# Optimization experiments

Measured on AMD Instinct MI355X. Metric: run time of the kernel, lower is better.

## Reference

```python
import jax, jax.numpy as jnp
import numpy as np

BS, NQ, NC = 8, 100, 81      # batch, queries, classes (COCO-like)
M = 160                      # total targets across batch (20 per image)
H = W = 256                  # mask resolution
P = H * W                    # pixels per mask

COST_CLASS = 1.0
COST_MASK = 1.0
COST_DICE = 1.0


def setup_inputs() -> dict:
    key = jax.random.key(0)
    k1, k2, k3, k4 = jax.random.split(key, 4)
    return {
        "pred_logits": jax.random.normal(k1, (BS, NQ, NC), dtype=jnp.float32),
        "pred_masks": jax.random.normal(k2, (BS, NQ, H, W), dtype=jnp.float32),
        "tgt_ids": jax.random.randint(k3, (M,), 0, NC),
        # binary ground-truth masks, flattened to [M, P]
        "tgt_mask": jnp.round(jax.random.uniform(k4, (M, P), dtype=jnp.float32)),
    }


def reference(pred_logits, pred_masks, tgt_ids, tgt_mask):
    bs, nq = pred_logits.shape[:2]
    N = bs * nq

    # ---- classification cost: -softmax(logits)[:, tgt_ids]  -> [N, M]
    out_prob = jax.nn.softmax(pred_logits.reshape(N, -1), axis=-1)
    cost_class = -out_prob[:, tgt_ids]

    x = pred_masks.reshape(N, -1)          # [N, P] mask logits
    t = tgt_mask                           # [M, P] binary targets
    p = x.shape[1]

    # ---- pairwise BCE-with-logits cost, mean over pixels.
    # bce(x, t) = max(x,0) - x*t + log1p(exp(-|x|)); mean_p splits into a
    # per-prediction row term minus a matmul cross term (avoids the N x M x P blowup).
    pos = jnp.maximum(x, 0.0) + jnp.log1p(jnp.exp(-jnp.abs(x)))   # [N, P]
    row = pos.sum(axis=1)                                          # [N]
    cross = x @ t.T                                                # [N, M]
    cost_mask = (row[:, None] - cross) / p

    # ---- pairwise dice cost: 1 - (2<s,t> + 1) / (sum s + sum t + 1)
    s = jax.nn.sigmoid(x)                                          # [N, P]
    numerator = 2.0 * (s @ t.T)                                    # [N, M]
    denominator = s.sum(axis=1)[:, None] + t.sum(axis=1)[None, :]  # [N, M]
    cost_dice = 1.0 - (numerator + 1.0) / (denominator + 1.0)

    C = COST_CLASS * cost_class + COST_MASK * cost_mask + COST_DICE * cost_dice
    return C.reshape(bs, nq, -1)           # [bs, nq, M] cost matrix
```

## Files before the change

### kernel.cpp

```cpp
#include <hip/hip_runtime.h>
#include <cmath>

#define NROWS 800
#define NCLS  81
#define MT    160
#define PPX   65536
#define SSPLIT 32
#define CHUNK 2048
#define BK    64
#define ITERS (CHUNK / BK)
#define RPB   32
#define RB    25

#define OFF_TBF   0
#define SZ_TBF    (MT * PPX * 2)
#define OFF_CROSS (SZ_TBF)
#define OFF_SDOT  (OFF_CROSS + NROWS * MT * 4)
#define OFF_ROW   (OFF_SDOT + NROWS * MT * 4)
#define OFF_SSUM  (OFF_ROW + NROWS * 4)
#define OFF_TSUM  (OFF_SSUM + NROWS * 4)
#define OFF_PROB  (OFF_TSUM + MT * 4)
#define OFF_END   (OFF_PROB + NROWS * NCLS * 4)

typedef __attribute__((ext_vector_type(8))) short bf16x8;
typedef __attribute__((ext_vector_type(4))) float f32x4;

typedef __attribute__((address_space(3))) char lds_char;
typedef const __attribute__((address_space(1))) char glob_char;

__device__ __forceinline__ unsigned short f2bf(float f) {
    unsigned int u = __float_as_uint(f);
    unsigned int r = (u + 0x7FFFu + ((u >> 16) & 1u)) >> 16;
    return (unsigned short)r;
}

__global__ __launch_bounds__(256) void prep_kernel(const float* __restrict__ tgt_mask,
                                                   char* __restrict__ ws) {
    int g = blockIdx.x * 256 + threadIdx.x;
    int m = g >> 13;
    int kc = g & 8191;
    const float4* src = (const float4*)(tgt_mask + (size_t)m * PPX + (kc << 3));
    float4 a = src[0], b = src[1];
    float part = a.x + a.y + a.z + a.w + b.x + b.y + b.z + b.w;

    uint4 o;
    o.x = (unsigned)f2bf(a.x) | ((unsigned)f2bf(a.y) << 16);
    o.y = (unsigned)f2bf(a.z) | ((unsigned)f2bf(a.w) << 16);
    o.z = (unsigned)f2bf(b.x) | ((unsigned)f2bf(b.y) << 16);
    o.w = (unsigned)f2bf(b.z) | ((unsigned)f2bf(b.w) << 16);

    int group = kc >> 3;
    int c = kc & 7;
    int oc = (group << 3) | (c ^ (m & 7));
    *(uint4*)(ws + OFF_TBF + (size_t)m * (PPX * 2) + (size_t)oc * 16) = o;

    #pragma unroll
    for (int mk = 32; mk; mk >>= 1) part += __shfl_xor(part, mk);
    __shared__ float wsum[4];
    if ((threadIdx.x & 63) == 0) wsum[threadIdx.x >> 6] = part;
    __syncthreads();
    if (threadIdx.x == 0) {
        float tot = wsum[0] + wsum[1] + wsum[2] + wsum[3];
        atomicAdd((float*)(ws + OFF_TSUM) + m, tot);
    }
}

__global__ __launch_bounds__(64) void softmax_kernel(const float* __restrict__ logits,
                                                     float* __restrict__ prob) {
    int n = blockIdx.x;
    int l = threadIdx.x;
    const float* row = logits + n * NCLS;
    float v0 = row[l];
    float v1 = (l + 64 < NCLS) ? row[l + 64] : -INFINITY;
    float mx = fmaxf(v0, v1);
    #pragma unroll
    for (int mk = 32; mk; mk >>= 1) mx = fmaxf(mx, __shfl_xor(mx, mk));
    float e0 = __expf(v0 - mx);
    float e1 = (l + 64 < NCLS) ? __expf(v1 - mx) : 0.f;
    float s = e0 + e1;
    #pragma unroll
    for (int mk = 32; mk; mk >>= 1) s += __shfl_xor(s, mk);
    float inv = 1.f / s;
    prob[n * NCLS + l] = e0 * inv;
    if (l + 64 < NCLS) prob[n * NCLS + l + 64] = e1 * inv;
}

struct XS { float4 a; float4 b; };

__device__ __forceinline__ void loadx(XS& x, const float* xrow, int it) {
    const float* p = xrow + it * BK;
    x.a = *(const float4*)(p);
    x.b = *(const float4*)(p + 4);
}

__device__ __forceinline__ void ew8(const XS& xs, bf16x8& xv, bf16x8& sv,
                                    float& slog2, float& sg_acc) {
    float vals[8] = {xs.a.x, xs.a.y, xs.a.z, xs.a.w, xs.b.x, xs.b.y, xs.b.z, xs.b.w};
    #pragma unroll
    for (int j = 0; j < 8; ++j) {
        float v = vals[j];
        float vl = fminf(v * 1.44269504089f, 126.f);
        float t2 = __builtin_amdgcn_exp2f(vl);
        float d = 1.f + t2;
        float r = __builtin_amdgcn_rcpf(d);
        float sg = t2 * r;
        slog2 += __builtin_amdgcn_logf(d);
        sg_acc += sg;
        xv[j] = (short)f2bf(v);
        sv[j] = (short)f2bf(sg);
    }
}

__global__ __launch_bounds__(256) void main_kernel(const float* __restrict__ pred_masks,
                                                   char* __restrict__ ws) {
    __shared__ __align__(16) unsigned short lds_t[2][MT * BK];
    __shared__ __align__(16) unsigned short lds_x[RPB * BK];
    __shared__ __align__(16) unsigned short lds_s[RPB * BK];

    const int tid = threadIdx.x;
    const int w = tid >> 6, l = tid & 63;
    const int rb = blockIdx.x >> 5;
    const int s = blockIdx.x & 31;
    const int k_base = s * CHUNK;

    const int srow = tid >> 3;
    const int sc8 = tid & 7;
    const int n_glob = rb * RPB + srow;
    const float* xrow = pred_masks + (size_t)n_glob * PPX + k_base + sc8 * 8;
    char* xw = (char*)lds_x + srow * 128 + ((sc8 ^ (srow & 7)) * 16);
    char* swp = (char*)lds_s + srow * 128 + ((sc8 ^ (srow & 7)) * 16);

    const char* tbase = ws + OFF_TBF;

    auto stage_t = [&](int b, int tt) {
        const int k0 = k_base + tt * BK;
        #pragma unroll
        for (int i = 0; i < 5; ++i) {
            int rows_base = w * 40 + i * 8;
            const char* g = (const char*)tbase
                          + (size_t)(rows_base + (l >> 3)) * (PPX * 2)
                          + (size_t)k0 * 2 + (size_t)(l & 7) * 16;
            __builtin_amdgcn_global_load_lds((glob_char*)g,
                                             (lds_char*)((char*)lds_t[b] + rows_base * 128),
                                             16, 0, 0);
        }
    };

    const int wr = w & 1, wc = w >> 1;
    f32x4 accX[5], accS[5];
    #pragma unroll
    for (int i = 0; i < 5; ++i) { accX[i] = (f32x4)(0.f); accS[i] = (f32x4)(0.f); }
    float slog2 = 0.f, rs_sg = 0.f;

    stage_t(0, 0);
    XS XA, XB;
    loadx(XA, xrow, 0);
    loadx(XB, xrow, 1);

    #pragma unroll 1
    for (int it = 0; it < ITERS; it += 2) {
        #pragma unroll
        for (int half = 0; half < 2; ++half) {
            const int h = it + half;
            const int hb = half;

            int tn = h + 1; if (tn >= ITERS) tn = ITERS - 1;
            stage_t(hb ^ 1, tn);
            __builtin_amdgcn_sched_barrier(0);

            bf16x8 xv, sv;
            if (half == 0) ew8(XA, xv, sv, slog2, rs_sg);
            else           ew8(XB, xv, sv, slog2, rs_sg);
            *(bf16x8*)xw = xv;
            *(bf16x8*)swp = sv;

            int tr = h + 2; if (tr >= ITERS) tr = ITERS - 1;
            if (half == 0) loadx(XA, xrow, tr);
            else           loadx(XB, xrow, tr);

            asm volatile("s_waitcnt vmcnt(9) lgkmcnt(0)" ::: "memory");
            __builtin_amdgcn_sched_barrier(0);
            __builtin_amdgcn_s_barrier();
            __builtin_amdgcn_sched_barrier(0);

            #pragma unroll
            for (int kk = 0; kk < 2; ++kk) {
                int arow = wr * 16 + (l & 15);
                int achunk = (kk * 4 + (l >> 4)) ^ (arow & 7);
                bf16x8 ax = *(bf16x8*)((char*)lds_x + arow * 128 + achunk * 16);
                bf16x8 as = *(bf16x8*)((char*)lds_s + arow * 128 + achunk * 16);
                #pragma unroll
                for (int cf = 0; cf < 5; ++cf) {
                    int mrow = (wc * 5 + cf) * 16 + (l & 15);
                    int bchunk = (kk * 4 + (l >> 4)) ^ (mrow & 7);
                    bf16x8 bv = *(bf16x8*)((char*)lds_t[hb] + mrow * 128 + bchunk * 16);
                    accX[cf] = __builtin_amdgcn_mfma_f32_16x16x32_bf16(ax, bv, accX[cf], 0, 0, 0);
                    accS[cf] = __builtin_amdgcn_mfma_f32_16x16x32_bf16(as, bv, accS[cf], 0, 0, 0);
                }
            }

            asm volatile("s_waitcnt lgkmcnt(0)" ::: "memory");
            __builtin_amdgcn_sched_barrier(0);
            __builtin_amdgcn_s_barrier();
            __builtin_amdgcn_sched_barrier(0);
        }
    }

    asm volatile("s_waitcnt vmcnt(0)" ::: "memory");

    float rs_sp = slog2 * 0.69314718056f;
    rs_sp += __shfl_xor(rs_sp, 1); rs_sp += __shfl_xor(rs_sp, 2); rs_sp += __shfl_xor(rs_sp, 4);
    rs_sg += __shfl_xor(rs_sg, 1); rs_sg += __shfl_xor(rs_sg, 2); rs_sg += __shfl_xor(rs_sg, 4);
    float* acc_row = (float*)(ws + OFF_ROW);
    float* acc_ssum = (float*)(ws + OFF_SSUM);
    if ((tid & 7) == 0) {
        atomicAdd(acc_row + n_glob, rs_sp);
        atomicAdd(acc_ssum + n_glob, rs_sg);
    }

    float* acc_cross = (float*)(ws + OFF_CROSS);
    float* acc_sdot = (float*)(ws + OFF_SDOT);
    #pragma unroll
    for (int cf = 0; cf < 5; ++cf) {
        int mcol = (wc * 5 + cf) * 16 + (l & 15);
        #pragma unroll
        for (int i = 0; i < 4; ++i) {
            int nrow = rb * RPB + wr * 16 + (l >> 4) * 4 + i;
            atomicAdd(acc_cross + nrow * MT + mcol, accX[cf][i]);
            atomicAdd(acc_sdot + nrow * MT + mcol, accS[cf][i]);
        }
    }
}

__global__ __launch_bounds__(256) void final_kernel(const int* __restrict__ tgt_ids,
                                                    const char* __restrict__ ws,
                                                    float* __restrict__ out) {
    int idx = blockIdx.x * 256 + threadIdx.x;
    int n = idx / MT;
    int m = idx - n * MT;
    const float* prob = (const float*)(ws + OFF_PROB);
    const float* acc_cross = (const float*)(ws + OFF_CROSS);
    const float* acc_sdot = (const float*)(ws + OFF_SDOT);
    const float* acc_row = (const float*)(ws + OFF_ROW);
    const float* acc_ssum = (const float*)(ws + OFF_SSUM);
    const float* tsum = (const float*)(ws + OFF_TSUM);

    float cls = -prob[n * NCLS + tgt_ids[m]];
    float cmask = (acc_row[n] - acc_cross[idx]) * (1.f / PPX);
    float cdice = 1.f - (2.f * acc_sdot[idx] + 1.f) / (acc_ssum[n] + tsum[m] + 1.f);
    out[idx] = cls + cmask + cdice;
}

extern "C" void kernel_launch(void* const* d_in, const int* in_sizes, int n_in,
                              void* d_out, int out_size, void* d_ws, size_t ws_size,
                              hipStream_t stream) {
    const float* pred_logits = (const float*)d_in[0];
    const float* pred_masks  = (const float*)d_in[1];
    const int*   tgt_ids     = (const int*)d_in[2];
    const float* tgt_mask    = (const float*)d_in[3];
    char* ws = (char*)d_ws;

    (void)hipMemsetAsync(ws + OFF_CROSS, 0, OFF_END - OFF_CROSS, stream);
    prep_kernel<<<5120, 256, 0, stream>>>(tgt_mask, ws);
    softmax_kernel<<<NROWS, 64, 0, stream>>>(pred_logits, (float*)(ws + OFF_PROB));
    main_kernel<<<RB * SSPLIT, 256, 0, stream>>>(pred_masks, ws);
    final_kernel<<<500, 256, 0, stream>>>(tgt_ids, ws, (float*)d_out);
}
```

Before: 137.4 us.

## Load target mask fragments directly into registers instead of staging through LDS

The bf16 target matrix is no longer staged through a double-buffered LDS tile with global_load_lds. Each wave now loads its B-operand fragments straight from global memory into registers, prefetching one step ahead, and covers 3 column tiles across both row tiles. The last wave's third tile is clamped and its work is thrown away. The LDS now holds only double-buffered x and sigmoid tiles, and the prep kernel drops the XOR swizzle. The goal is to cut LDS traffic, LDS footprint and one barrier per step, at the cost of more register pressure, uncoalesced 16-byte global loads, and about 20% redundant MFMA work.

```diff
diff --git a/kernel.cpp b/kernel.cpp
--- a/kernel.cpp
+++ b/kernel.cpp
@@ -25,9 +25,6 @@
 typedef __attribute__((ext_vector_type(8))) short bf16x8;
 typedef __attribute__((ext_vector_type(4))) float f32x4;
 
-typedef __attribute__((address_space(3))) char lds_char;
-typedef const __attribute__((address_space(1))) char glob_char;
-
 __device__ __forceinline__ unsigned short f2bf(float f) {
     unsigned int u = __float_as_uint(f);
     unsigned int r = (u + 0x7FFFu + ((u >> 16) & 1u)) >> 16;
@@ -48,11 +45,7 @@
     o.y = (unsigned)f2bf(a.z) | ((unsigned)f2bf(a.w) << 16);
     o.z = (unsigned)f2bf(b.x) | ((unsigned)f2bf(b.y) << 16);
     o.w = (unsigned)f2bf(b.z) | ((unsigned)f2bf(b.w) << 16);
-
-    int group = kc >> 3;
-    int c = kc & 7;
-    int oc = (group << 3) | (c ^ (m & 7));
-    *(uint4*)(ws + OFF_TBF + (size_t)m * (PPX * 2) + (size_t)oc * 16) = o;
+    *(uint4*)(ws + OFF_TBF + (size_t)m * (PPX * 2) + (size_t)kc * 16) = o;
 
     #pragma unroll
     for (int mk = 32; mk; mk >>= 1) part += __shfl_xor(part, mk);
@@ -113,9 +106,8 @@
 
 __global__ __launch_bounds__(256) void main_kernel(const float* __restrict__ pred_masks,
                                                    char* __restrict__ ws) {
-    __shared__ __align__(16) unsigned short lds_t[2][MT * BK];
-    __shared__ __align__(16) unsigned short lds_x[RPB * BK];
-    __shared__ __align__(16) unsigned short lds_s[RPB * BK];
+    __shared__ __align__(16) unsigned short lds_x[2][RPB * BK];
+    __shared__ __align__(16) unsigned short lds_s[2][RPB * BK];
 
     const int tid = threadIdx.x;
     const int w = tid >> 6, l = tid & 63;
@@ -127,82 +119,108 @@
     const int sc8 = tid & 7;
     const int n_glob = rb * RPB + srow;
     const float* xrow = pred_masks + (size_t)n_glob * PPX + k_base + sc8 * 8;
-    char* xw = (char*)lds_x + srow * 128 + ((sc8 ^ (srow & 7)) * 16);
-    char* swp = (char*)lds_s + srow * 128 + ((sc8 ^ (srow & 7)) * 16);
-
-    const char* tbase = ws + OFF_TBF;
-
-    auto stage_t = [&](int b, int tt) {
-        const int k0 = k_base + tt * BK;
+    const int xoff = srow * 128 + ((sc8 ^ (srow & 7)) * 16);
+
+    const unsigned short* tb = (const unsigned short*)(ws + OFF_TBF);
+    const int lrow = l & 15;
+    const int lk8 = (l >> 4) * 8;
+    const unsigned short* tp[3];
+    #pragma unroll
+    for (int c = 0; c < 3; ++c) {
+        int ctile = 3 * w + c;
+        int crow = (ctile < 10 ? ctile : 9) * 16 + lrow;
+        tp[c] = tb + (size_t)crow * PPX + k_base + lk8;
+    }
+
+    f32x4 accX[2][3], accS[2][3];
+    #pragma unroll
+    for (int rt = 0; rt < 2; ++rt)
         #pragma unroll
-        for (int i = 0; i < 5; ++i) {
-            int rows_base = w * 40 + i * 8;
-            const char* g = (const char*)tbase
-                          + (size_t)(rows_base + (l >> 3)) * (PPX * 2)
-                          + (size_t)k0 * 2 + (size_t)(l & 7) * 16;
-            __builtin_amdgcn_global_load_lds((glob_char*)g,
-                                             (lds_char*)((char*)lds_t[b] + rows_base * 128),
-                                             16, 0, 0);
-        }
-    };
-
-    const int wr = w & 1, wc = w >> 1;
-    f32x4 accX[5], accS[5];
-    #pragma unroll
-    for (int i = 0; i < 5; ++i) { accX[i] = (f32x4)(0.f); accS[i] = (f32x4)(0.f); }
+        for (int c = 0; c < 3; ++c) { accX[rt][c] = (f32x4)(0.f); accS[rt][c] = (f32x4)(0.f); }
     float slog2 = 0.f, rs_sg = 0.f;
 
-    stage_t(0, 0);
+    bf16x8 TA[2][3], TB[2][3];
     XS XA, XB;
+
+    #pragma unroll
+    for (int kk = 0; kk < 2; ++kk)
+        #pragma unroll
+        for (int c = 0; c < 3; ++c)
+            TA[kk][c] = *(const bf16x8*)(tp[c] + kk * 32);
     loadx(XA, xrow, 0);
     loadx(XB, xrow, 1);
 
     #pragma unroll 1
     for (int it = 0; it < ITERS; it += 2) {
-        #pragma unroll
-        for (int half = 0; half < 2; ++half) {
-            const int h = it + half;
-            const int hb = half;
-
-            int tn = h + 1; if (tn >= ITERS) tn = ITERS - 1;
-            stage_t(hb ^ 1, tn);
-            __builtin_amdgcn_sched_barrier(0);
-
+        {
             bf16x8 xv, sv;
-            if (half == 0) ew8(XA, xv, sv, slog2, rs_sg);
-            else           ew8(XB, xv, sv, slog2, rs_sg);
-            *(bf16x8*)xw = xv;
-            *(bf16x8*)swp = sv;
-
-            int tr = h + 2; if (tr >= ITERS) tr = ITERS - 1;
-            if (half == 0) loadx(XA, xrow, tr);
-            else           loadx(XB, xrow, tr);
-
-            asm volatile("s_waitcnt vmcnt(9) lgkmcnt(0)" ::: "memory");
+            ew8(XA, xv, sv, slog2, rs_sg);
+            *(bf16x8*)((char*)lds_x[0] + xoff) = xv;
+            *(bf16x8*)((char*)lds_s[0] + xoff) = sv;
+            asm volatile("s_waitcnt lgkmcnt(0)" ::: "memory");
             __builtin_amdgcn_sched_barrier(0);
             __builtin_amdgcn_s_barrier();
             __builtin_amdgcn_sched_barrier(0);
 
-            #pragma unroll
-            for (int kk = 0; kk < 2; ++kk) {
-                int arow = wr * 16 + (l & 15);
-                int achunk = (kk * 4 + (l >> 4)) ^ (arow & 7);
-                bf16x8 ax = *(bf16x8*)((char*)lds_x + arow * 128 + achunk * 16);
-                bf16x8 as = *(bf16x8*)((char*)lds_s + arow * 128 + achunk * 16);
-                #pragma unroll
-                for (int cf = 0; cf < 5; ++cf) {
-                    int mrow = (wc * 5 + cf) * 16 + (l & 15);
-                    int bchunk = (kk * 4 + (l >> 4)) ^ (mrow & 7);
-                    bf16x8 bv = *(bf16x8*)((char*)lds_t[hb] + mrow * 128 + bchunk * 16);
-                    accX[cf] = __builtin_amdgcn_mfma_f32_16x16x32_bf16(ax, bv, accX[cf], 0, 0, 0);
-                    accS[cf] = __builtin_amdgcn_mfma_f32_16x16x32_bf16(as, bv, accS[cf], 0, 0, 0);
+            const int tn = it + 1;
+            #pragma unroll
+            for (int kk = 0; kk < 2; ++kk)
+                #pragma unroll
+                for (int c = 0; c < 3; ++c)
+                    TB[kk][c] = *(const bf16x8*)(tp[c] + tn * BK + kk * 32);
+            int tr = it + 2; if (tr >= ITERS) tr = ITERS - 1;
+            loadx(XA, xrow, tr);
+            __builtin_amdgcn_sched_barrier(0);
+
+            #pragma unroll
+            for (int rt = 0; rt < 2; ++rt)
+                #pragma unroll
+                for (int kk = 0; kk < 2; ++kk) {
+                    const int arow = rt * 16 + lrow;
+                    const int achunk = (kk * 4 + (l >> 4)) ^ (arow & 7);
+                    bf16x8 ax = *(bf16x8*)((char*)lds_x[0] + arow * 128 + achunk * 16);
+                    bf16x8 as_ = *(bf16x8*)((char*)lds_s[0] + arow * 128 + achunk * 16);
+                    #pragma unroll
+                    for (int c = 0; c < 3; ++c) {
+                        accX[rt][c] = __builtin_amdgcn_mfma_f32_16x16x32_bf16(ax, TA[kk][c], accX[rt][c], 0, 0, 0);
+                        accS[rt][c] = __builtin_amdgcn_mfma_f32_16x16x32_bf16(as_, TA[kk][c], accS[rt][c], 0, 0, 0);
+                    }
                 }
-            }
-
+        }
+        {
+            bf16x8 xv, sv;
+            ew8(XB, xv, sv, slog2, rs_sg);
+            *(bf16x8*)((char*)lds_x[1] + xoff) = xv;
+            *(bf16x8*)((char*)lds_s[1] + xoff) = sv;
             asm volatile("s_waitcnt lgkmcnt(0)" ::: "memory");
             __builtin_amdgcn_sched_barrier(0);
             __builtin_amdgcn_s_barrier();
             __builtin_amdgcn_sched_barrier(0);
+
+            int tn = it + 2; if (tn >= ITERS) tn = ITERS - 1;
+            #pragma unroll
+            for (int kk = 0; kk < 2; ++kk)
+                #pragma unroll
+                for (int c = 0; c < 3; ++c)
+                    TA[kk][c] = *(const bf16x8*)(tp[c] + tn * BK + kk * 32);
+            int tr = it + 3; if (tr >= ITERS) tr = ITERS - 1;
+            loadx(XB, xrow, tr);
+            __builtin_amdgcn_sched_barrier(0);
+
+            #pragma unroll
+            for (int rt = 0; rt < 2; ++rt)
+                #pragma unroll
+                for (int kk = 0; kk < 2; ++kk) {
+                    const int arow = rt * 16 + lrow;
+                    const int achunk = (kk * 4 + (l >> 4)) ^ (arow & 7);
+                    bf16x8 ax = *(bf16x8*)((char*)lds_x[1] + arow * 128 + achunk * 16);
+                    bf16x8 as_ = *(bf16x8*)((char*)lds_s[1] + arow * 128 + achunk * 16);
+                    #pragma unroll
+                    for (int c = 0; c < 3; ++c) {
+                        accX[rt][c] = __builtin_amdgcn_mfma_f32_16x16x32_bf16(ax, TB[kk][c], accX[rt][c], 0, 0, 0);
+                        accS[rt][c] = __builtin_amdgcn_mfma_f32_16x16x32_bf16(as_, TB[kk][c], accS[rt][c], 0, 0, 0);
+                    }
+                }
         }
     }
 
@@ -221,15 +239,20 @@
     float* acc_cross = (float*)(ws + OFF_CROSS);
     float* acc_sdot = (float*)(ws + OFF_SDOT);
     #pragma unroll
-    for (int cf = 0; cf < 5; ++cf) {
-        int mcol = (wc * 5 + cf) * 16 + (l & 15);
+    for (int rt = 0; rt < 2; ++rt)
         #pragma unroll
-        for (int i = 0; i < 4; ++i) {
-            int nrow = rb * RPB + wr * 16 + (l >> 4) * 4 + i;
-            atomicAdd(acc_cross + nrow * MT + mcol, accX[cf][i]);
-            atomicAdd(acc_sdot + nrow * MT + mcol, accS[cf][i]);
+        for (int c = 0; c < 3; ++c) {
+            int ctile = 3 * w + c;
+            if (ctile < 10) {
+                int mcol = ctile * 16 + lrow;
+                #pragma unroll
+                for (int i = 0; i < 4; ++i) {
+                    int nrow = rb * RPB + rt * 16 + (l >> 4) * 4 + i;
+                    atomicAdd(acc_cross + nrow * MT + mcol, accX[rt][c][i]);
+                    atomicAdd(acc_sdot + nrow * MT + mcol, accS[rt][c][i]);
+                }
+            }
         }
-    }
 }
 
 __global__ __launch_bounds__(256) void final_kernel(const int* __restrict__ tgt_ids,
```

Result: slower. 153.0 us (+11.4%).

## Double rows per block and drop target-tile double buffering

Applied to the files above, without the earlier changes.

Each block of the main GEMM kernel now covers 64 prediction rows instead of 32, using two 16-row MFMA tiles per wave. Each block works on a smaller pixel chunk, with the split-K factor going from 32 to 64. This roughly halves how often the bf16 target masks are re-read across row blocks and reuses each staged target tile across more rows. In exchange, the target tile in LDS is single-buffered and loaded at the start of each step, so its load latency is no longer hidden behind the previous step's MFMAs. The grid is padded to 832 rows, with guarded loads and atomics, so some compute is wasted on dummy rows.

```diff
diff --git a/kernel.cpp b/kernel.cpp
--- a/kernel.cpp
+++ b/kernel.cpp
@@ -5,12 +5,12 @@
 #define NCLS  81
 #define MT    160
 #define PPX   65536
-#define SSPLIT 32
-#define CHUNK 2048
+#define SSPLIT 64
+#define CHUNK 1024
 #define BK    64
 #define ITERS (CHUNK / BK)
-#define RPB   32
-#define RB    25
+#define RPB   64
+#define RBLK  13
 
 #define OFF_TBF   0
 #define SZ_TBF    (MT * PPX * 2)
@@ -85,54 +85,58 @@
     if (l + 64 < NCLS) prob[n * NCLS + l + 64] = e1 * inv;
 }
 
-struct XS { float4 a; float4 b; };
+struct XS { float4 a, b, c, d; };
 
 __device__ __forceinline__ void loadx(XS& x, const float* xrow, int it) {
     const float* p = xrow + it * BK;
     x.a = *(const float4*)(p);
     x.b = *(const float4*)(p + 4);
-}
-
-__device__ __forceinline__ void ew8(const XS& xs, bf16x8& xv, bf16x8& sv,
+    x.c = *(const float4*)(p + 8);
+    x.d = *(const float4*)(p + 12);
+}
+
+__device__ __forceinline__ void ew8(const float4& u, const float4& v,
+                                    bf16x8& xv, bf16x8& sv,
                                     float& slog2, float& sg_acc) {
-    float vals[8] = {xs.a.x, xs.a.y, xs.a.z, xs.a.w, xs.b.x, xs.b.y, xs.b.z, xs.b.w};
+    float vals[8] = {u.x, u.y, u.z, u.w, v.x, v.y, v.z, v.w};
     #pragma unroll
     for (int j = 0; j < 8; ++j) {
-        float v = vals[j];
-        float vl = fminf(v * 1.44269504089f, 126.f);
+        float t = vals[j];
+        float vl = fminf(t * 1.44269504089f, 126.f);
         float t2 = __builtin_amdgcn_exp2f(vl);
         float d = 1.f + t2;
         float r = __builtin_amdgcn_rcpf(d);
         float sg = t2 * r;
         slog2 += __builtin_amdgcn_logf(d);
         sg_acc += sg;
-        xv[j] = (short)f2bf(v);
+        xv[j] = (short)f2bf(t);
         sv[j] = (short)f2bf(sg);
     }
 }
 
 __global__ __launch_bounds__(256) void main_kernel(const float* __restrict__ pred_masks,
                                                    char* __restrict__ ws) {
-    __shared__ __align__(16) unsigned short lds_t[2][MT * BK];
+    __shared__ __align__(16) unsigned short lds_t[MT * BK];
     __shared__ __align__(16) unsigned short lds_x[RPB * BK];
     __shared__ __align__(16) unsigned short lds_s[RPB * BK];
 
     const int tid = threadIdx.x;
     const int w = tid >> 6, l = tid & 63;
-    const int rb = blockIdx.x >> 5;
-    const int s = blockIdx.x & 31;
+    const int rb = blockIdx.x >> 6;
+    const int s = blockIdx.x & 63;
     const int k_base = s * CHUNK;
 
-    const int srow = tid >> 3;
-    const int sc8 = tid & 7;
+    const int srow = tid >> 2;
+    const int q = tid & 3;
     const int n_glob = rb * RPB + srow;
-    const float* xrow = pred_masks + (size_t)n_glob * PPX + k_base + sc8 * 8;
-    char* xw = (char*)lds_x + srow * 128 + ((sc8 ^ (srow & 7)) * 16);
-    char* swp = (char*)lds_s + srow * 128 + ((sc8 ^ (srow & 7)) * 16);
+    const int n_safe = n_glob < NROWS ? n_glob : NROWS - 1;
+    const float* xrow = pred_masks + (size_t)n_safe * PPX + k_base + q * 16;
+    const int xo0 = srow * 128 + (((2 * q + 0) ^ (srow & 7)) * 16);
+    const int xo1 = srow * 128 + (((2 * q + 1) ^ (srow & 7)) * 16);
 
     const char* tbase = ws + OFF_TBF;
 
-    auto stage_t = [&](int b, int tt) {
+    auto stage_t = [&](int tt) {
         const int k0 = k_base + tt * BK;
         #pragma unroll
         for (int i = 0; i < 5; ++i) {
@@ -141,18 +145,20 @@
                           + (size_t)(rows_base + (l >> 3)) * (PPX * 2)
                           + (size_t)k0 * 2 + (size_t)(l & 7) * 16;
             __builtin_amdgcn_global_load_lds((glob_char*)g,
-                                             (lds_char*)((char*)lds_t[b] + rows_base * 128),
+                                             (lds_char*)((char*)lds_t + rows_base * 128),
                                              16, 0, 0);
         }
     };
 
     const int wr = w & 1, wc = w >> 1;
-    f32x4 accX[5], accS[5];
-    #pragma unroll
-    for (int i = 0; i < 5; ++i) { accX[i] = (f32x4)(0.f); accS[i] = (f32x4)(0.f); }
+    const int lrow = l & 15;
+    f32x4 accX[2][5], accS[2][5];
+    #pragma unroll
+    for (int rt = 0; rt < 2; ++rt)
+        #pragma unroll
+        for (int c = 0; c < 5; ++c) { accX[rt][c] = (f32x4)(0.f); accS[rt][c] = (f32x4)(0.f); }
     float slog2 = 0.f, rs_sg = 0.f;
 
-    stage_t(0, 0);
     XS XA, XB;
     loadx(XA, xrow, 0);
     loadx(XB, xrow, 1);
@@ -162,74 +168,80 @@
         #pragma unroll
         for (int half = 0; half < 2; ++half) {
             const int h = it + half;
-            const int hb = half;
-
-            int tn = h + 1; if (tn >= ITERS) tn = ITERS - 1;
-            stage_t(hb ^ 1, tn);
-            __builtin_amdgcn_sched_barrier(0);
-
-            bf16x8 xv, sv;
-            if (half == 0) ew8(XA, xv, sv, slog2, rs_sg);
-            else           ew8(XB, xv, sv, slog2, rs_sg);
-            *(bf16x8*)xw = xv;
-            *(bf16x8*)swp = sv;
+            stage_t(h);
+
+            bf16x8 xv0, sv0, xv1, sv1;
+            if (half == 0) { ew8(XA.a, XA.b, xv0, sv0, slog2, rs_sg);
+                             ew8(XA.c, XA.d, xv1, sv1, slog2, rs_sg); }
+            else           { ew8(XB.a, XB.b, xv0, sv0, slog2, rs_sg);
+                             ew8(XB.c, XB.d, xv1, sv1, slog2, rs_sg); }
+            *(bf16x8*)((char*)lds_x + xo0) = xv0;
+            *(bf16x8*)((char*)lds_x + xo1) = xv1;
+            *(bf16x8*)((char*)lds_s + xo0) = sv0;
+            *(bf16x8*)((char*)lds_s + xo1) = sv1;
 
             int tr = h + 2; if (tr >= ITERS) tr = ITERS - 1;
             if (half == 0) loadx(XA, xrow, tr);
             else           loadx(XB, xrow, tr);
 
-            asm volatile("s_waitcnt vmcnt(9) lgkmcnt(0)" ::: "memory");
+            asm volatile("s_waitcnt vmcnt(4) lgkmcnt(0)" ::: "memory");
             __builtin_amdgcn_sched_barrier(0);
             __builtin_amdgcn_s_barrier();
             __builtin_amdgcn_sched_barrier(0);
 
             #pragma unroll
-            for (int kk = 0; kk < 2; ++kk) {
-                int arow = wr * 16 + (l & 15);
-                int achunk = (kk * 4 + (l >> 4)) ^ (arow & 7);
-                bf16x8 ax = *(bf16x8*)((char*)lds_x + arow * 128 + achunk * 16);
-                bf16x8 as = *(bf16x8*)((char*)lds_s + arow * 128 + achunk * 16);
+            for (int rt = 0; rt < 2; ++rt)
                 #pragma unroll
-                for (int cf = 0; cf < 5; ++cf) {
-                    int mrow = (wc * 5 + cf) * 16 + (l & 15);
-                    int bchunk = (kk * 4 + (l >> 4)) ^ (mrow & 7);
-                    bf16x8 bv = *(bf16x8*)((char*)lds_t[hb] + mrow * 128 + bchunk * 16);
-                    accX[cf] = __builtin_amdgcn_mfma_f32_16x16x32_bf16(ax, bv, accX[cf], 0, 0, 0);
-                    accS[cf] = __builtin_amdgcn_mfma_f32_16x16x32_bf16(as, bv, accS[cf], 0, 0, 0);
+                for (int kk = 0; kk < 2; ++kk) {
+                    const int arow = wr * 32 + rt * 16 + lrow;
+                    const int achunk = (kk * 4 + (l >> 4)) ^ (arow & 7);
+                    bf16x8 ax = *(bf16x8*)((char*)lds_x + arow * 128 + achunk * 16);
+                    bf16x8 as_ = *(bf16x8*)((char*)lds_s + arow * 128 + achunk * 16);
+                    #pragma unroll
+                    for (int cf = 0; cf < 5; ++cf) {
+                        const int mrow = (wc * 5 + cf) * 16 + lrow;
+                        const int bchunk = (kk * 4 + (l >> 4)) ^ (mrow & 7);
+                        bf16x8 bv = *(bf16x8*)((char*)lds_t + mrow * 128 + bchunk * 16);
+                        accX[rt][cf] = __builtin_amdgcn_mfma_f32_16x16x32_bf16(ax, bv, accX[rt][cf], 0, 0, 0);
+                        accS[rt][cf] = __builtin_amdgcn_mfma_f32_16x16x32_bf16(as_, bv, accS[rt][cf], 0, 0, 0);
+                    }
+                }
+
+            asm volatile("s_waitcnt lgkmcnt(0)" ::: "memory");
+            __builtin_amdgcn_sched_barrier(0);
+            __builtin_amdgcn_s_barrier();
+            __builtin_amdgcn_sched_barrier(0);
+        }
+    }
+
+    asm volatile("s_waitcnt vmcnt(0)" ::: "memory");
+
+    float rs_sp = slog2 * 0.69314718056f;
+    rs_sp += __shfl_xor(rs_sp, 1); rs_sp += __shfl_xor(rs_sp, 2);
+    rs_sg += __shfl_xor(rs_sg, 1); rs_sg += __shfl_xor(rs_sg, 2);
+    float* acc_row = (float*)(ws + OFF_ROW);
+    float* acc_ssum = (float*)(ws + OFF_SSUM);
+    if ((tid & 3) == 0 && n_glob < NROWS) {
+        atomicAdd(acc_row + n_glob, rs_sp);
+        atomicAdd(acc_ssum + n_glob, rs_sg);
+    }
+
+    float* acc_cross = (float*)(ws + OFF_CROSS);
+    float* acc_sdot = (float*)(ws + OFF_SDOT);
+    #pragma unroll
+    for (int rt = 0; rt < 2; ++rt)
+        #pragma unroll
+        for (int cf = 0; cf < 5; ++cf) {
+            int mcol = (wc * 5 + cf) * 16 + lrow;
+            #pragma unroll
+            for (int i = 0; i < 4; ++i) {
+                int nrow = rb * RPB + wr * 32 + rt * 16 + (l >> 4) * 4 + i;
+                if (nrow < NROWS) {
+                    atomicAdd(acc_cross + nrow * MT + mcol, accX[rt][cf][i]);
+                    atomicAdd(acc_sdot + nrow * MT + mcol, accS[rt][cf][i]);
                 }
             }
-
-            asm volatile("s_waitcnt lgkmcnt(0)" ::: "memory");
-            __builtin_amdgcn_sched_barrier(0);
-            __builtin_amdgcn_s_barrier();
-            __builtin_amdgcn_sched_barrier(0);
         }
-    }
-
-    asm volatile("s_waitcnt vmcnt(0)" ::: "memory");
-
-    float rs_sp = slog2 * 0.69314718056f;
-    rs_sp += __shfl_xor(rs_sp, 1); rs_sp += __shfl_xor(rs_sp, 2); rs_sp += __shfl_xor(rs_sp, 4);
-    rs_sg += __shfl_xor(rs_sg, 1); rs_sg += __shfl_xor(rs_sg, 2); rs_sg += __shfl_xor(rs_sg, 4);
-    float* acc_row = (float*)(ws + OFF_ROW);
-    float* acc_ssum = (float*)(ws + OFF_SSUM);
-    if ((tid & 7) == 0) {
-        atomicAdd(acc_row + n_glob, rs_sp);
-        atomicAdd(acc_ssum + n_glob, rs_sg);
-    }
-
-    float* acc_cross = (float*)(ws + OFF_CROSS);
-    float* acc_sdot = (float*)(ws + OFF_SDOT);
-    #pragma unroll
-    for (int cf = 0; cf < 5; ++cf) {
-        int mcol = (wc * 5 + cf) * 16 + (l & 15);
-        #pragma unroll
-        for (int i = 0; i < 4; ++i) {
-            int nrow = rb * RPB + wr * 16 + (l >> 4) * 4 + i;
-            atomicAdd(acc_cross + nrow * MT + mcol, accX[cf][i]);
-            atomicAdd(acc_sdot + nrow * MT + mcol, accS[cf][i]);
-        }
-    }
 }
 
 __global__ __launch_bounds__(256) void final_kernel(const int* __restrict__ tgt_ids,
@@ -263,6 +275,6 @@
     (void)hipMemsetAsync(ws + OFF_CROSS, 0, OFF_END - OFF_CROSS, stream);
     prep_kernel<<<5120, 256, 0, stream>>>(tgt_mask, ws);
     softmax_kernel<<<NROWS, 64, 0, stream>>>(pred_logits, (float*)(ws + OFF_PROB));
-    main_kernel<<<RB * SSPLIT, 256, 0, stream>>>(pred_masks, ws);
+    main_kernel<<<RBLK * SSPLIT, 256, 0, stream>>>(pred_masks, ws);
     final_kernel<<<500, 256, 0, stream>>>(tgt_ids, ws, (float*)d_out);
 }
```

Result: slower. 178.1 us (+29.6%).

## Switch mask matmuls from bf16 to fp8 MFMA with doubled K step

Applied to the files above, without the earlier changes.

Converts the binary target masks, the mask logits and the sigmoid values to FP8 (e4m3) instead of bf16, and uses the fp8 16x16x32 MFMA. This halves the footprint of the target workspace and the LDS staging traffic. The K step per iteration doubles to 128 and the target tile drops from double buffering to a single LDS buffer. The risks are a large loss of precision in the cross and dot terms from FP8 logits, and less overlap between the target loads and the MFMA work.

```diff
diff --git a/kernel.cpp b/kernel.cpp
--- a/kernel.cpp
+++ b/kernel.cpp
@@ -7,13 +7,13 @@
 #define PPX   65536
 #define SSPLIT 32
 #define CHUNK 2048
-#define BK    64
-#define ITERS (CHUNK / BK)
+#define BK    128
+#define STEPS (CHUNK / BK)
 #define RPB   32
 #define RB    25
 
 #define OFF_TBF   0
-#define SZ_TBF    (MT * PPX * 2)
+#define SZ_TBF    (MT * PPX)
 #define OFF_CROSS (SZ_TBF)
 #define OFF_SDOT  (OFF_CROSS + NROWS * MT * 4)
 #define OFF_ROW   (OFF_SDOT + NROWS * MT * 4)
@@ -22,17 +22,11 @@
 #define OFF_PROB  (OFF_TSUM + MT * 4)
 #define OFF_END   (OFF_PROB + NROWS * NCLS * 4)
 
-typedef __attribute__((ext_vector_type(8))) short bf16x8;
 typedef __attribute__((ext_vector_type(4))) float f32x4;
+typedef long i64;
 
 typedef __attribute__((address_space(3))) char lds_char;
 typedef const __attribute__((address_space(1))) char glob_char;
-
-__device__ __forceinline__ unsigned short f2bf(float f) {
-    unsigned int u = __float_as_uint(f);
-    unsigned int r = (u + 0x7FFFu + ((u >> 16) & 1u)) >> 16;
-    return (unsigned short)r;
-}
 
 __global__ __launch_bounds__(256) void prep_kernel(const float* __restrict__ tgt_mask,
                                                    char* __restrict__ ws) {
@@ -43,16 +37,17 @@
     float4 a = src[0], b = src[1];
     float part = a.x + a.y + a.z + a.w + b.x + b.y + b.z + b.w;
 
-    uint4 o;
-    o.x = (unsigned)f2bf(a.x) | ((unsigned)f2bf(a.y) << 16);
-    o.y = (unsigned)f2bf(a.z) | ((unsigned)f2bf(a.w) << 16);
-    o.z = (unsigned)f2bf(b.x) | ((unsigned)f2bf(b.y) << 16);
-    o.w = (unsigned)f2bf(b.z) | ((unsigned)f2bf(b.w) << 16);
-
-    int group = kc >> 3;
-    int c = kc & 7;
-    int oc = (group << 3) | (c ^ (m & 7));
-    *(uint4*)(ws + OFF_TBF + (size_t)m * (PPX * 2) + (size_t)oc * 16) = o;
+    unsigned w0 = __builtin_amdgcn_cvt_pk_fp8_f32(a.x, a.y, 0, false);
+    w0 = __builtin_amdgcn_cvt_pk_fp8_f32(a.z, a.w, w0, true);
+    unsigned w1 = __builtin_amdgcn_cvt_pk_fp8_f32(b.x, b.y, 0, false);
+    w1 = __builtin_amdgcn_cvt_pk_fp8_f32(b.z, b.w, w1, true);
+
+    int group = kc >> 4;
+    int c = (kc >> 1) & 7;
+    int h = kc & 1;
+    uint2 o; o.x = w0; o.y = w1;
+    *(uint2*)(ws + OFF_TBF + (size_t)m * PPX + (size_t)group * 128
+              + (size_t)(c ^ (m & 7)) * 16 + h * 8) = o;
 
     #pragma unroll
     for (int mk = 32; mk; mk >>= 1) part += __shfl_xor(part, mk);
@@ -85,37 +80,41 @@
     if (l + 64 < NCLS) prob[n * NCLS + l + 64] = e1 * inv;
 }
 
-struct XS { float4 a; float4 b; };
-
-__device__ __forceinline__ void loadx(XS& x, const float* xrow, int it) {
-    const float* p = xrow + it * BK;
+struct XS4 { float4 a, b, c, d; };
+
+__device__ __forceinline__ void loadx(XS4& x, const float* xrow, int st) {
+    const float* p = xrow + st * BK;
     x.a = *(const float4*)(p);
     x.b = *(const float4*)(p + 4);
-}
-
-__device__ __forceinline__ void ew8(const XS& xs, bf16x8& xv, bf16x8& sv,
+    x.c = *(const float4*)(p + 8);
+    x.d = *(const float4*)(p + 12);
+}
+
+__device__ __forceinline__ void ew4(const float4 v, unsigned& wx, unsigned& ws_,
                                     float& slog2, float& sg_acc) {
-    float vals[8] = {xs.a.x, xs.a.y, xs.a.z, xs.a.w, xs.b.x, xs.b.y, xs.b.z, xs.b.w};
-    #pragma unroll
-    for (int j = 0; j < 8; ++j) {
-        float v = vals[j];
-        float vl = fminf(v * 1.44269504089f, 126.f);
+    float s[4]; float vals[4] = {v.x, v.y, v.z, v.w};
+    #pragma unroll
+    for (int j = 0; j < 4; ++j) {
+        float t = vals[j];
+        float vl = fminf(t * 1.44269504089f, 126.f);
         float t2 = __builtin_amdgcn_exp2f(vl);
         float d = 1.f + t2;
         float r = __builtin_amdgcn_rcpf(d);
-        float sg = t2 * r;
+        s[j] = t2 * r;
         slog2 += __builtin_amdgcn_logf(d);
-        sg_acc += sg;
-        xv[j] = (short)f2bf(v);
-        sv[j] = (short)f2bf(sg);
-    }
+        sg_acc += s[j];
+    }
+    wx = __builtin_amdgcn_cvt_pk_fp8_f32(vals[0], vals[1], 0, false);
+    wx = __builtin_amdgcn_cvt_pk_fp8_f32(vals[2], vals[3], wx, true);
+    ws_ = __builtin_amdgcn_cvt_pk_fp8_f32(s[0], s[1], 0, false);
+    ws_ = __builtin_amdgcn_cvt_pk_fp8_f32(s[2], s[3], ws_, true);
 }
 
 __global__ __launch_bounds__(256) void main_kernel(const float* __restrict__ pred_masks,
                                                    char* __restrict__ ws) {
-    __shared__ __align__(16) unsigned short lds_t[2][MT * BK];
-    __shared__ __align__(16) unsigned short lds_x[RPB * BK];
-    __shared__ __align__(16) unsigned short lds_s[RPB * BK];
+    __shared__ __align__(16) char lds_t[MT * BK];
+    __shared__ __align__(16) char lds_x[RPB * BK];
+    __shared__ __align__(16) char lds_s[RPB * BK];
 
     const int tid = threadIdx.x;
     const int w = tid >> 6, l = tid & 63;
@@ -123,79 +122,87 @@
     const int s = blockIdx.x & 31;
     const int k_base = s * CHUNK;
 
-    const int srow = tid >> 3;
-    const int sc8 = tid & 7;
-    const int n_glob = rb * RPB + srow;
-    const float* xrow = pred_masks + (size_t)n_glob * PPX + k_base + sc8 * 8;
-    char* xw = (char*)lds_x + srow * 128 + ((sc8 ^ (srow & 7)) * 16);
-    char* swp = (char*)lds_s + srow * 128 + ((sc8 ^ (srow & 7)) * 16);
+    const int row = tid >> 3;
+    const int c8 = tid & 7;
+    const int n_glob = rb * RPB + row;
+    const float* xrow = pred_masks + (size_t)n_glob * PPX + k_base + c8 * 16;
+    char* xw = lds_x + row * 128 + ((c8 ^ (row & 7)) * 16);
+    char* swp = lds_s + row * 128 + ((c8 ^ (row & 7)) * 16);
 
     const char* tbase = ws + OFF_TBF;
 
-    auto stage_t = [&](int b, int tt) {
-        const int k0 = k_base + tt * BK;
+    auto stage_t = [&](int st) {
+        const size_t k0 = k_base + st * BK;
         #pragma unroll
         for (int i = 0; i < 5; ++i) {
             int rows_base = w * 40 + i * 8;
-            const char* g = (const char*)tbase
-                          + (size_t)(rows_base + (l >> 3)) * (PPX * 2)
-                          + (size_t)k0 * 2 + (size_t)(l & 7) * 16;
+            const char* g = tbase + (size_t)(rows_base + (l >> 3)) * PPX
+                          + k0 + (size_t)(l & 7) * 16;
             __builtin_amdgcn_global_load_lds((glob_char*)g,
-                                             (lds_char*)((char*)lds_t[b] + rows_base * 128),
+                                             (lds_char*)(lds_t + rows_base * 128),
                                              16, 0, 0);
         }
     };
 
     const int wr = w & 1, wc = w >> 1;
+    const int lrow = l & 15;
+    const int inner8 = ((l >> 4) & 1) * 8;
+    const int cpair = (l >> 4) >> 1;
     f32x4 accX[5], accS[5];
     #pragma unroll
     for (int i = 0; i < 5; ++i) { accX[i] = (f32x4)(0.f); accS[i] = (f32x4)(0.f); }
     float slog2 = 0.f, rs_sg = 0.f;
 
-    stage_t(0, 0);
-    XS XA, XB;
+    XS4 XA, XB;
     loadx(XA, xrow, 0);
     loadx(XB, xrow, 1);
 
     #pragma unroll 1
-    for (int it = 0; it < ITERS; it += 2) {
+    for (int it = 0; it < STEPS; it += 2) {
         #pragma unroll
         for (int half = 0; half < 2; ++half) {
             const int h = it + half;
-            const int hb = half;
-
-            int tn = h + 1; if (tn >= ITERS) tn = ITERS - 1;
-            stage_t(hb ^ 1, tn);
-            __builtin_amdgcn_sched_barrier(0);
-
-            bf16x8 xv, sv;
-            if (half == 0) ew8(XA, xv, sv, slog2, rs_sg);
-            else           ew8(XB, xv, sv, slog2, rs_sg);
-            *(bf16x8*)xw = xv;
-            *(bf16x8*)swp = sv;
-
-            int tr = h + 2; if (tr >= ITERS) tr = ITERS - 1;
+            stage_t(h);
+            __builtin_amdgcn_sched_barrier(0);
+
+            uint4 vx, vs;
+            if (half == 0) {
+                ew4(XA.a, vx.x, vs.x, slog2, rs_sg);
+                ew4(XA.b, vx.y, vs.y, slog2, rs_sg);
+                ew4(XA.c, vx.z, vs.z, slog2, rs_sg);
+                ew4(XA.d, vx.w, vs.w, slog2, rs_sg);
+            } else {
+                ew4(XB.a, vx.x, vs.x, slog2, rs_sg);
+                ew4(XB.b, vx.y, vs.y, slog2, rs_sg);
+                ew4(XB.c, vx.z, vs.z, slog2, rs_sg);
+                ew4(XB.d, vx.w, vs.w, slog2, rs_sg);
+            }
+            *(uint4*)xw = vx;
+            *(uint4*)swp = vs;
+
+            int tr = h + 2; if (tr >= STEPS) tr = STEPS - 1;
             if (half == 0) loadx(XA, xrow, tr);
             else           loadx(XB, xrow, tr);
 
-            asm volatile("s_waitcnt vmcnt(9) lgkmcnt(0)" ::: "memory");
+            __builtin_amdgcn_sched_barrier(0);
+            asm volatile("s_waitcnt vmcnt(4) lgkmcnt(0)" ::: "memory");
             __builtin_amdgcn_sched_barrier(0);
             __builtin_amdgcn_s_barrier();
             __builtin_amdgcn_sched_barrier(0);
 
             #pragma unroll
-            for (int kk = 0; kk < 2; ++kk) {
-                int arow = wr * 16 + (l & 15);
-                int achunk = (kk * 4 + (l >> 4)) ^ (arow & 7);
-                bf16x8 ax = *(bf16x8*)((char*)lds_x + arow * 128 + achunk * 16);
-                bf16x8 as = *(bf16x8*)((char*)lds_s + arow * 128 + achunk * 16);
+            for (int ks = 0; ks < 4; ++ks) {
+                const int arow = wr * 16 + lrow;
+                const int ac = (2 * ks + cpair) ^ (arow & 7);
+                i64 ax = *(const i64*)(lds_x + arow * 128 + ac * 16 + inner8);
+                i64 as_ = *(const i64*)(lds_s + arow * 128 + ac * 16 + inner8);
                 #pragma unroll
                 for (int cf = 0; cf < 5; ++cf) {
-                    int mrow = (wc * 5 + cf) * 16 + (l & 15);
-                    int bchunk = (kk * 4 + (l >> 4)) ^ (mrow & 7);
-                    bf16x8 bv = *(bf16x8*)((char*)lds_t[hb] + mrow * 128 + bchunk * 16);
-                    accX[cf] = __builtin_amdgcn_mfma_f32_16x16x32_bf16(ax, bv, accX[cf], 0, 0, 0);
-                    accS[cf] = __builtin_amdgcn_mfma_f32_16x16x32_bf16(as, bv, accS[cf], 0, 0, 0);
+                    const int mrow = (wc * 5 + cf) * 16 + lrow;
+                    const int bc = (2 * ks + cpair) ^ (mrow & 7);
+                    i64 bv = *(const i64*)(lds_t + mrow * 128 + bc * 16 + inner8);
+                    accX[cf] = __builtin_amdgcn_mfma_f32_16x16x32_fp8_fp8(ax, bv, accX[cf], 0, 0, 0);
+                    accS[cf] = __builtin_amdgcn_mfma_f32_16x16x32_fp8_fp8(as_, bv, accS[cf], 0, 0, 0);
                 }
             }
 
@@ -222,7 +229,7 @@
     float* acc_sdot = (float*)(ws + OFF_SDOT);
     #pragma unroll
     for (int cf = 0; cf < 5; ++cf) {
-        int mcol = (wc * 5 + cf) * 16 + (l & 15);
+        int mcol = (wc * 5 + cf) * 16 + lrow;
         #pragma unroll
         for (int i = 0; i < 4; ++i) {
             int nrow = rb * RPB + wr * 16 + (l >> 4) * 4 + i;
```

New measurement: 117.1 us. -14.8%, faster.
